# Optimization experiments

Measured on AMD Instinct MI355X. Metric: run time of the kernel, lower is better.

Reference implementation:

```python
import jax, jax.numpy as jnp
import numpy as np

N = 50000      # nodes
D = 16         # fixed in-degree per node
E = N * D      # edges
C = 128        # in_channels == hidden_channels
H = 128        # hidden_channels
ED = 16        # edge_dim
OUT = 2        # out_channels


def setup_inputs() -> dict:
    key = jax.random.key(0)
    ks = jax.random.split(key, 16)
    s = 0.05
    x = jax.random.normal(ks[0], (N, C), jnp.float32)
    src = jax.random.randint(ks[1], (E,), 0, N)
    dst = jnp.repeat(jnp.arange(N), D)           # sorted by destination, degree D each
    edge_index = jnp.stack([src, dst]).astype(jnp.int32)
    edge_attr = jax.random.normal(ks[2], (E, ED), jnp.float32)
    # 3 SAGEConv layers, each: LSTM(C->C) aggregator + lin_l(C->H, bias) + lin_r(C->H, no bias)
    Wih = jax.random.normal(ks[3], (3, 4 * C, C), jnp.float32) * s
    Whh = jax.random.normal(ks[4], (3, 4 * C, C), jnp.float32) * s
    bih = jax.random.normal(ks[5], (3, 4 * C), jnp.float32) * s
    bhh = jax.random.normal(ks[6], (3, 4 * C), jnp.float32) * s
    lin_l_W = jax.random.normal(ks[7], (3, H, C), jnp.float32) * s
    lin_l_b = jax.random.normal(ks[8], (3, H), jnp.float32) * s
    lin_r_W = jax.random.normal(ks[9], (3, H, C), jnp.float32) * s
    # edge MLP: (2H+ED)->H->H//2->OUT
    W1 = jax.random.normal(ks[10], (H, 2 * H + ED), jnp.float32) * s
    b1 = jax.random.normal(ks[11], (H,), jnp.float32) * s
    W2 = jax.random.normal(ks[12], (H // 2, H), jnp.float32) * s
    b2 = jax.random.normal(ks[13], (H // 2,), jnp.float32) * s
    W3 = jax.random.normal(ks[14], (OUT, H // 2), jnp.float32) * s
    b3 = jax.random.normal(ks[15], (OUT,), jnp.float32) * s
    return dict(x=x, edge_index=edge_index, edge_attr=edge_attr,
                Wih=Wih, Whh=Whh, bih=bih, bhh=bhh,
                lin_l_W=lin_l_W, lin_l_b=lin_l_b, lin_r_W=lin_r_W,
                W1=W1, b1=b1, W2=W2, b2=b2, W3=W3, b3=b3)


def _lstm_last(seq, wih, whh, bi, bh):
    # seq: [N, D, C] -> last LSTM output [N, C] (torch gate order i,f,g,o)
    h0 = jnp.zeros((seq.shape[0], whh.shape[1]), seq.dtype)

    def step(carry, xt):
        h, c = carry
        gates = xt @ wih.T + bi + h @ whh.T + bh
        i, f, g, o = jnp.split(gates, 4, axis=-1)
        c = jax.nn.sigmoid(f) * c + jax.nn.sigmoid(i) * jnp.tanh(g)
        h = jax.nn.sigmoid(o) * jnp.tanh(c)
        return (h, c), None

    (h, _), _ = jax.lax.scan(step, (h0, h0), seq.transpose(1, 0, 2))
    return h


def _sage_lstm(x, src, wih, whh, bi, bh, wl, bl, wr):
    # fixed degree D, edges sorted by dst -> group-by-dst is a reshape
    seq = x[src].reshape(N, D, -1)           # [N, D, C] neighbor sequences
    agg = _lstm_last(seq, wih, whh, bi, bh)  # [N, C]
    return agg @ wl.T + bl + x @ wr.T        # lin_l(agg) + lin_r(x)


def reference(x, edge_index, edge_attr, Wih, Whh, bih, bhh,
              lin_l_W, lin_l_b, lin_r_W, W1, b1, W2, b2, W3, b3):
    src, dst = edge_index[0], edge_index[1]
    h = x
    for l in range(3):
        h = jax.nn.relu(_sage_lstm(h, src, Wih[l], Whh[l], bih[l], bhh[l],
                                   lin_l_W[l], lin_l_b[l], lin_r_W[l]))
    # gather-concat edge MLP (dropout is identity in eval)
    feat = jnp.concatenate([h[src], h[dst], edge_attr], axis=1)  # [E, 2H+ED]
    e = jax.nn.relu(feat @ W1.T + b1)
    e = jax.nn.relu(e @ W2.T + b2)
    return e @ W3.T + b3
```

## Files before the change

### kernel.cpp

```cpp
#include <hip/hip_runtime.h>
#include <hip/hip_bf16.h>

#define NN 50000
#define DEG 16

typedef __attribute__((ext_vector_type(8))) short bfrag;
typedef __attribute__((ext_vector_type(4))) float f32x4;

__device__ __forceinline__ float bf2f(unsigned int u){ return __uint_as_float(u<<16); }
__device__ __forceinline__ unsigned short f2bf(float x){
  unsigned int u = __float_as_uint(x);
  unsigned int r = (u + 0x7fffu + ((u>>16)&1u)) >> 16;
  return (unsigned short)r;
}
__device__ __forceinline__ float fast_rcp(float x){ return __builtin_amdgcn_rcpf(x); }
__device__ __forceinline__ float sigmoidf_(float x){ return fast_rcp(1.f + __expf(-x)); }
__device__ __forceinline__ float tanh_fast(float x){
  float e = __expf(-2.f*fabsf(x));
  float r = (1.f - e)*fast_rcp(1.f + e);
  return copysignf(r, x);
}

#define SWZ(row) (((((row) ^ ((row)>>3)) & 7)) << 4)
#define SW4(row) (((row) & 15) << 4)

#define GLDS16(g, l) __builtin_amdgcn_global_load_lds( \
    (const __attribute__((address_space(1))) unsigned int*)(g), \
    (__attribute__((address_space(3))) unsigned int*)(l), 16, 0, 0)

__global__ void k_cvt(const float* __restrict__ in, unsigned short* __restrict__ out, int n){
  int i = blockIdx.x*256 + threadIdx.x;
  if (i < n) out[i] = f2bf(in[i]);
}

__global__ void k_cvt2(const float* __restrict__ in, unsigned short* __restrict__ out,
                       int stride, int off, int cols, int total){
  int i = blockIdx.x*256 + threadIdx.x;
  if (i < total){
    int r = i / cols, c = i - r*cols;
    out[i] = f2bf(in[(size_t)r*stride + off + c]);
  }
}

__global__ void k_prep_lstm(const float* __restrict__ Wih, const float* __restrict__ Whh,
                            const float* __restrict__ bih, const float* __restrict__ bhh,
                            unsigned short* __restrict__ Wcat, float* __restrict__ bsum)
{
  int i = blockIdx.x*256 + threadIdx.x;
  if (i < 3*512*256){
    int l = i >> 17;
    int rem = i & 131071;
    int row = rem >> 8, col = rem & 255;
    float v = (col < 128) ? Wih[((size_t)l*512 + row)*128 + col]
                          : Whh[((size_t)l*512 + row)*128 + (col-128)];
    Wcat[i] = f2bf(v);
  } else if (i < 3*512*256 + 3*512){
    int k = i - 3*512*256;
    bsum[k] = bih[k] + bhh[k];
  }
}

__global__ void k_prep_edge(const float* __restrict__ W1, const float* __restrict__ W2,
                            const float* __restrict__ W3,
                            unsigned short* __restrict__ W1eh, unsigned short* __restrict__ W1el,
                            unsigned short* __restrict__ W2h, unsigned short* __restrict__ W2l,
                            unsigned short* __restrict__ W3p)
{
  int i = blockIdx.x*256 + threadIdx.x;
  if (i < 8192){
    float v = W2[i];
    unsigned short hi = f2bf(v);
    W2h[i] = hi; W2l[i] = f2bf(v - bf2f(hi));
  } else if (i < 10240){
    int k = i - 8192; int j = k >> 4, kk = k & 15;
    float v = W1[(size_t)j*272 + 256 + kk];
    unsigned short hi = f2bf(v);
    W1eh[k] = hi; W1el[k] = f2bf(v - bf2f(hi));
  } else if (i < 11264){
    int k = i - 10240; int nr = k >> 6, c = k & 63;
    W3p[k] = f2bf(nr < 2 ? W3[nr*64 + c] : 0.f);
  }
}

__global__ __launch_bounds__(256,4) void k_bgemm(
    const unsigned short* __restrict__ Ab, const unsigned short* __restrict__ A2b,
    const unsigned short* __restrict__ Wb, const unsigned short* __restrict__ W2b,
    const float* __restrict__ bias, const float* __restrict__ bias2,
    float* __restrict__ outF, unsigned short* __restrict__ outB,
    int ostride, int dorelu, int n)
{
  const int t  = threadIdx.x;
  const int w  = t >> 6;
  const int l  = t & 63;
  const int ln = l & 15, q = l >> 4;
  const int n0 = blockIdx.x*64;
  const int j0 = blockIdx.y*128 + w*32;

  int nodeM[4];
#pragma unroll
  for (int mt=0;mt<4;mt++){ int nd = n0 + mt*16 + ln; nodeM[mt] = nd < n ? nd : n-1; }

  f32x4 acc[4][2];
#pragma unroll
  for (int mt=0;mt<4;mt++)
#pragma unroll
    for (int nt=0;nt<2;nt++) acc[mt][nt] = (f32x4){0.f,0.f,0.f,0.f};

  auto pass = [&](const unsigned short* __restrict__ Ap, const unsigned short* __restrict__ Wp){
#pragma unroll
    for (int ks=0;ks<4;ks++){
      bfrag Af[4], Bf[2];
#pragma unroll
      for (int mt=0;mt<4;mt++)
        Af[mt] = *(const bfrag*)(Ap + (size_t)nodeM[mt]*128 + ks*32 + q*8);
#pragma unroll
      for (int nt=0;nt<2;nt++)
        Bf[nt] = *(const bfrag*)(Wp + (size_t)(j0 + nt*16 + ln)*128 + ks*32 + q*8);
#pragma unroll
      for (int mt=0;mt<4;mt++)
#pragma unroll
        for (int nt=0;nt<2;nt++)
          acc[mt][nt] = __builtin_amdgcn_mfma_f32_16x16x32_bf16(Af[mt], Bf[nt], acc[mt][nt], 0,0,0);
    }
  };
  pass(Ab, Wb);
  if (A2b) pass(A2b, W2b);

#pragma unroll
  for (int nt=0;nt<2;nt++){
    int j = j0 + nt*16 + ln;
    float bv = bias ? bias[j] : 0.f;
    if (bias2) bv += bias2[j];
#pragma unroll
    for (int mt=0;mt<4;mt++)
#pragma unroll
      for (int r=0;r<4;r++){
        int row = n0 + mt*16 + q*4 + r;
        if (row < n){
          float v = acc[mt][nt][r] + bv;
          if (dorelu) v = fmaxf(v, 0.f);
          if (outF) outF[(size_t)row*ostride + j] = v;
          if (outB) outB[(size_t)row*ostride + j] = f2bf(v);
        }
      }
  }
}

__global__ __launch_bounds__(512,2) void k_lstm9(
    const unsigned short* __restrict__ xin,
    const int* __restrict__ src,
    const unsigned short* __restrict__ Wcat,
    const float* __restrict__ bsum,
    const unsigned short* __restrict__ Wlb,
    const unsigned short* __restrict__ Wrb,
    const float* __restrict__ bl,
    unsigned short* __restrict__ hout,
    int n)
{
  __shared__ unsigned short hs[64*128];
  __shared__ unsigned short xbuf[2][64*128];
  __shared__ int srcs[64*16];
  const int t  = threadIdx.x;
  const int w  = t >> 6;
  const int l  = t & 63;
  const int ln = l & 15;
  const int q  = l >> 4;
  const int n0 = blockIdx.x * 64;

  for (int i = t; i < 1024; i += 512){
    int nl = i >> 4, st = i & 15;
    srcs[i] = (n0+nl < n) ? src[(size_t)(n0+nl)*16 + st] : 0;
  }

  bfrag A[4][8];
#pragma unroll
  for (int T=0;T<4;T++)
#pragma unroll
    for (int ks=0;ks<8;ks++)
      A[T][ks] = *(const bfrag*)(Wcat + (size_t)(T*128 + w*16 + ln)*256 + ks*32 + q*8);

  f32x4 bsv[4];
#pragma unroll
  for (int T=0;T<4;T++)
    bsv[T] = *(const f32x4*)(bsum + T*128 + w*16 + q*4);

  float c[4][4];
#pragma unroll
  for (int nt=0;nt<4;nt++)
#pragma unroll
    for (int r=0;r<4;r++) c[nt][r]=0.f;

  __syncthreads();

  auto stageX = [&](int step, int buf){
#pragma unroll
    for (int j=0;j<2;j++){
      int row  = w*8 + j*4 + (l>>4);
      int node = srcs[row*16 + step];
      const char* gsrc = (const char*)xin + (size_t)node*256 + (((l&15)*16) ^ SW4(row));
      char* ldst = (char*)&xbuf[buf][0] + (w*8 + j*4)*256;
      GLDS16(gsrc, ldst);
    }
  };

  stageX(0, 0);
  asm volatile("s_waitcnt vmcnt(0)" ::: "memory");
  __syncthreads();

  for (int step=0; step<16; step++){
    const int cur = step & 1;
    if (step < 15) stageX(step+1, cur^1);

#pragma unroll
    for (int p=0;p<2;p++){
      f32x4 acc[4][2];
#pragma unroll
      for (int T=0;T<4;T++)
#pragma unroll
        for (int ntl=0;ntl<2;ntl++) acc[T][ntl] = (f32x4){0.f,0.f,0.f,0.f};

#pragma unroll
      for (int ntl=0; ntl<2; ntl++){
        int node = p*32 + ntl*16 + ln;
        int swz  = SW4(node);
#pragma unroll
        for (int ks=0;ks<4;ks++){
          bfrag Bk = *(const bfrag*)((const char*)&xbuf[cur][0] + node*256 +
                       ((ks*64 + q*16) ^ swz));
#pragma unroll
          for (int T=0;T<4;T++)
            acc[T][ntl] = __builtin_amdgcn_mfma_f32_16x16x32_bf16(A[T][ks], Bk, acc[T][ntl], 0,0,0);
        }
        if (step > 0){
#pragma unroll
          for (int ks=4;ks<8;ks++){
            bfrag Bk = *(const bfrag*)((const char*)hs + node*256 +
                         (((ks-4)*64 + q*16) ^ swz));
#pragma unroll
            for (int T=0;T<4;T++)
              acc[T][ntl] = __builtin_amdgcn_mfma_f32_16x16x32_bf16(A[T][ks], Bk, acc[T][ntl], 0,0,0);
          }
        }
      }

      if (p == 1){
        asm volatile("s_waitcnt vmcnt(0)" ::: "memory");
      }
      __syncthreads();

#pragma unroll
      for (int ntl=0; ntl<2; ntl++){
        int nt = p*2 + ntl;
        int node = p*32 + ntl*16 + ln;
        float h[4];
#pragma unroll
        for (int r=0;r<4;r++){
          float iv = acc[0][ntl][r] + bsv[0][r];
          float fv = acc[1][ntl][r] + bsv[1][r];
          float gg = acc[2][ntl][r] + bsv[2][r];
          float ov = acc[3][ntl][r] + bsv[3][r];
          float cn = sigmoidf_(fv)*c[nt][r] + sigmoidf_(iv)*tanh_fast(gg);
          c[nt][r] = cn;
          h[r] = sigmoidf_(ov)*tanh_fast(cn);
        }
        unsigned pk01, pk23;
        asm("v_cvt_pk_bf16_f32 %0, %1, %2" : "=v"(pk01) : "v"(h[0]), "v"(h[1]));
        asm("v_cvt_pk_bf16_f32 %0, %1, %2" : "=v"(pk23) : "v"(h[2]), "v"(h[3]));
        uint2 pv; pv.x = pk01; pv.y = pk23;
        *(uint2*)((char*)hs + node*256 + (((w*32 + q*8)) ^ SW4(node))) = pv;
      }
    }
  }

  __syncthreads();
  {
    bfrag Al[4], Ar[4];
#pragma unroll
    for (int ks=0;ks<4;ks++){
      Al[ks] = *(const bfrag*)(Wlb + (size_t)(w*16+ln)*128 + ks*32 + q*8);
      Ar[ks] = *(const bfrag*)(Wrb + (size_t)(w*16+ln)*128 + ks*32 + q*8);
    }
    f32x4 blv = *(const f32x4*)(bl + w*16 + q*4);
#pragma unroll
    for (int nt=0; nt<4; nt++){
      int node = nt*16 + ln;
      int gn = (n0+node < n) ? (n0+node) : (n-1);
      f32x4 acc = (f32x4){0.f,0.f,0.f,0.f};
#pragma unroll
      for (int ks=0;ks<4;ks++){
        bfrag Bh = *(const bfrag*)((const char*)hs + node*256 +
                     ((ks*64 + q*16) ^ SW4(node)));
        bfrag Bx = *(const bfrag*)(xin + (size_t)gn*128 + ks*32 + q*8);
        acc = __builtin_amdgcn_mfma_f32_16x16x32_bf16(Al[ks], Bh, acc, 0,0,0);
        acc = __builtin_amdgcn_mfma_f32_16x16x32_bf16(Ar[ks], Bx, acc, 0,0,0);
      }
      float v0 = fmaxf(acc[0]+blv[0], 0.f), v1 = fmaxf(acc[1]+blv[1], 0.f);
      float v2 = fmaxf(acc[2]+blv[2], 0.f), v3 = fmaxf(acc[3]+blv[3], 0.f);
      unsigned pk01, pk23;
      asm("v_cvt_pk_bf16_f32 %0, %1, %2" : "=v"(pk01) : "v"(v0), "v"(v1));
      asm("v_cvt_pk_bf16_f32 %0, %1, %2" : "=v"(pk23) : "v"(v2), "v"(v3));
      if (n0+node < n){
        uint2 pv; pv.x = pk01; pv.y = pk23;
        *(uint2*)(hout + (size_t)(n0+node)*128 + w*16 + q*4) = pv;
      }
    }
  }
}

__global__ __launch_bounds__(256,2) void k_edge3(
    const float* __restrict__ HsHd,
    const float* __restrict__ ea,
    const int* __restrict__ src,
    const unsigned short* __restrict__ W1eh, const unsigned short* __restrict__ W1el,
    const unsigned short* __restrict__ W2h,  const unsigned short* __restrict__ W2l,
    const unsigned short* __restrict__ W3p,
    const float* __restrict__ b1, const float* __restrict__ b2, const float* __restrict__ b3,
    float* __restrict__ out)
{
  __shared__ unsigned short out1h[64*128];
  __shared__ unsigned short out1l[64*128];
  __shared__ unsigned short e2h[64*64];
  __shared__ unsigned short e2l[64*64];
  __shared__ unsigned short ea2[64*56];

  const int t = threadIdx.x;
  const int w = t>>6, l = t&63, ln = l&15, q = l>>4;
  const int nblk = blockIdx.x;
  const size_t e0 = (size_t)nblk*64;

  int srcv[4];
#pragma unroll
  for (int r=0;r<4;r++) srcv[r] = src[e0 + w*16 + q*4 + r];

  float hsv[8][4];
#pragma unroll
  for (int nt=0;nt<8;nt++)
#pragma unroll
    for (int r=0;r<4;r++)
      hsv[nt][r] = HsHd[(size_t)srcv[r]*256 + nt*16 + ln];

  float hdv[8];
#pragma unroll
  for (int nt=0;nt<8;nt++)
    hdv[nt] = HsHd[((size_t)nblk*4 + w)*256 + 128 + nt*16 + ln];

  float b1v[8];
#pragma unroll
  for (int nt=0;nt<8;nt++) b1v[nt] = b1[nt*16 + ln];
  float b2v[4];
#pragma unroll
  for (int nt=0;nt<4;nt++) b2v[nt] = b2[nt*16 + ln];
  float b3v = (ln<2) ? b3[ln] : 0.f;

  bfrag w1h[8], w1l[8];
#pragma unroll
  for (int nt=0;nt<8;nt++){
    int j = nt*16 + ln;
    w1h[nt] = *(const bfrag*)(W1eh + (size_t)j*16 + (q&1)*8);
    w1l[nt] = *(const bfrag*)(W1el + (size_t)j*16 + (q&1)*8);
  }
  bfrag w3f[2];
#pragma unroll
  for (int ks=0;ks<2;ks++)
    w3f[ks] = *(const bfrag*)(W3p + (size_t)ln*64 + ks*32 + q*8);

  for (int i=t;i<1024;i+=256){
    int e=i>>4, k=i&15;
    float v = ea[(e0+e)*16 + k];
    unsigned short hi = f2bf(v);
    ea2[e*56 + k] = hi;
    ea2[e*56 + 16 + k] = f2bf(v - bf2f(hi));
  }
  __syncthreads();

  {
    bfrag Aea = *(const bfrag*)&ea2[(w*16+ln)*56 + q*8];
#pragma unroll
    for (int nt=0;nt<8;nt++){
      f32x4 acc;
#pragma unroll
      for (int r=0;r<4;r++) acc[r] = b1v[nt] + hdv[nt] + hsv[nt][r];
      acc = __builtin_amdgcn_mfma_f32_16x16x32_bf16(Aea, w1h[nt], acc, 0,0,0);
      acc = __builtin_amdgcn_mfma_f32_16x16x32_bf16(Aea, w1l[nt], acc, 0,0,0);
      int j = nt*16 + ln;
#pragma unroll
      for (int r=0;r<4;r++){
        int row = w*16 + q*4 + r;
        float v = fmaxf(acc[r], 0.f);
        unsigned short hi = f2bf(v);
        float lo = v - bf2f(hi);
        int byt = row*256 + ((j*2) ^ SWZ(row));
        *(unsigned short*)((char*)out1h + byt) = hi;
        *(unsigned short*)((char*)out1l + byt) = f2bf(lo);
      }
    }
  }
  __syncthreads();

  {
    f32x4 acc[4];
#pragma unroll
    for (int nt=0;nt<4;nt++) acc[nt] = (f32x4){b2v[nt],b2v[nt],b2v[nt],b2v[nt]};
    int arow = w*16 + ln;

    bfrag BhA[4], BlA[4], BhB[4], BlB[4];
#pragma unroll
    for (int nt=0;nt<4;nt++){
      int j = nt*16 + ln;
      BhA[nt] = *(const bfrag*)(W2h + (size_t)j*128 + q*8);
      BlA[nt] = *(const bfrag*)(W2l + (size_t)j*128 + q*8);
    }
#pragma unroll
    for (int ks=0;ks<4;ks++){
      if (ks < 3){
#pragma unroll
        for (int nt=0;nt<4;nt++){
          int j = nt*16 + ln;
          if ((ks&1)==0){
            BhB[nt] = *(const bfrag*)(W2h + (size_t)j*128 + (ks+1)*32 + q*8);
            BlB[nt] = *(const bfrag*)(W2l + (size_t)j*128 + (ks+1)*32 + q*8);
          } else {
            BhA[nt] = *(const bfrag*)(W2h + (size_t)j*128 + (ks+1)*32 + q*8);
            BlA[nt] = *(const bfrag*)(W2l + (size_t)j*128 + (ks+1)*32 + q*8);
          }
        }
      }
      int byt = arow*256 + ((ks*64 + q*16) ^ SWZ(arow));
      bfrag Ah = *(const bfrag*)((char*)out1h + byt);
      bfrag Al = *(const bfrag*)((char*)out1l + byt);
#pragma unroll
      for (int nt=0;nt<4;nt++){
        bfrag Bh = ((ks&1)==0) ? BhA[nt] : BhB[nt];
        bfrag Bl = ((ks&1)==0) ? BlA[nt] : BlB[nt];
        acc[nt] = __builtin_amdgcn_mfma_f32_16x16x32_bf16(Ah, Bh, acc[nt], 0,0,0);
        acc[nt] = __builtin_amdgcn_mfma_f32_16x16x32_bf16(Al, Bh, acc[nt], 0,0,0);
        acc[nt] = __builtin_amdgcn_mfma_f32_16x16x32_bf16(Ah, Bl, acc[nt], 0,0,0);
      }
    }
#pragma unroll
    for (int nt=0;nt<4;nt++)
#pragma unroll
      for (int r=0;r<4;r++){
        int row = w*16 + q*4 + r;
        int j = nt*16 + ln;
        float v = fmaxf(acc[nt][r], 0.f);
        unsigned short hi = f2bf(v);
        float lo = v - bf2f(hi);
        int byt = row*128 + ((j*2) ^ SWZ(row));
        *(unsigned short*)((char*)e2h + byt) = hi;
        *(unsigned short*)((char*)e2l + byt) = f2bf(lo);
      }
  }
  __syncthreads();

  {
    f32x4 acc = (f32x4){b3v,b3v,b3v,b3v};
    int arow = w*16 + ln;
#pragma unroll
    for (int ks=0;ks<2;ks++){
      int byt = arow*128 + ((ks*64 + q*16) ^ SWZ(arow));
      bfrag Ah = *(const bfrag*)((char*)e2h + byt);
      bfrag Al = *(const bfrag*)((char*)e2l + byt);
      acc = __builtin_amdgcn_mfma_f32_16x16x32_bf16(Ah, w3f[ks], acc, 0,0,0);
      acc = __builtin_amdgcn_mfma_f32_16x16x32_bf16(Al, w3f[ks], acc, 0,0,0);
    }
    if (ln < 2){
#pragma unroll
      for (int r=0;r<4;r++){
        int row = w*16 + q*4 + r;
        out[(e0 + row)*2 + ln] = acc[r];
      }
    }
  }
}

extern "C" void kernel_launch(void* const* d_in, const int* in_sizes, int n_in,
                              void* d_out, int out_size, void* d_ws, size_t ws_size,
                              hipStream_t stream) {
  const float* x    = (const float*)d_in[0];
  const int*   eidx = (const int*)  d_in[1];
  const float* eatt = (const float*)d_in[2];
  const float* Wih  = (const float*)d_in[3];
  const float* Whh  = (const float*)d_in[4];
  const float* bih  = (const float*)d_in[5];
  const float* bhh  = (const float*)d_in[6];
  const float* WlL  = (const float*)d_in[7];
  const float* blL  = (const float*)d_in[8];
  const float* WrL  = (const float*)d_in[9];
  const float* W1   = (const float*)d_in[10];
  const float* b1   = (const float*)d_in[11];
  const float* W2   = (const float*)d_in[12];
  const float* b2   = (const float*)d_in[13];
  const float* W3   = (const float*)d_in[14];
  const float* b3   = (const float*)d_in[15];
  const int*   src  = eidx;

  char* p = (char*)d_ws;
  float* HsHd        = (float*)p;
  p += (size_t)NN*512*2;
  unsigned short* xb   = (unsigned short*)p; p += (size_t)NN*128*2;
  unsigned short* hb1  = (unsigned short*)p; p += (size_t)NN*128*2;
  unsigned short* hb2  = (unsigned short*)p; p += (size_t)NN*128*2;
  unsigned short* Wcat = (unsigned short*)p; p += (size_t)3*512*256*2;
  float* bsum          = (float*)p;          p += (size_t)3*512*4;
  unsigned short* Wlb  = (unsigned short*)p; p += (size_t)3*128*128*2;
  unsigned short* Wrb  = (unsigned short*)p; p += (size_t)3*128*128*2;
  unsigned short* W1nb = (unsigned short*)p; p += (size_t)256*128*2;
  unsigned short* W1eh = (unsigned short*)p; p += 2048*2;
  unsigned short* W1el = (unsigned short*)p; p += 2048*2;
  unsigned short* W2h  = (unsigned short*)p; p += 8192*2;
  unsigned short* W2l  = (unsigned short*)p; p += 8192*2;
  unsigned short* W3p  = (unsigned short*)p; p += 1024*2;

  dim3 blk(256);
  const int nb = (NN + 63)/64;

  k_cvt<<<(NN*128+255)/256, blk, 0, stream>>>(x, xb, NN*128);
  k_prep_lstm<<<(3*512*256 + 3*512 + 255)/256, blk, 0, stream>>>(Wih, Whh, bih, bhh, Wcat, bsum);
  k_cvt<<<(3*128*128+255)/256, blk, 0, stream>>>(WlL, Wlb, 3*128*128);
  k_cvt<<<(3*128*128+255)/256, blk, 0, stream>>>(WrL, Wrb, 3*128*128);
  k_cvt2<<<(128*128+255)/256, blk, 0, stream>>>(W1, W1nb,           272, 0,   128, 128*128);
  k_cvt2<<<(128*128+255)/256, blk, 0, stream>>>(W1, W1nb+128*128,   272, 128, 128, 128*128);
  k_prep_edge<<<(11264+255)/256, blk, 0, stream>>>(W1, W2, W3, W1eh, W1el, W2h, W2l, W3p);

  const unsigned short* hin = xb;
  unsigned short* houts[3] = {hb1, hb2, hb1};
  for (int l = 0; l < 3; l++){
    k_lstm9<<<dim3(nb),dim3(512),0,stream>>>(hin, src,
        Wcat + (size_t)l*512*256, bsum + (size_t)l*512,
        Wlb + (size_t)l*128*128, Wrb + (size_t)l*128*128, blL + (size_t)l*128,
        houts[l], NN);
    hin = houts[l];
  }
  k_bgemm<<<dim3(nb,2),blk,0,stream>>>(hin, nullptr, W1nb, nullptr,
                                       nullptr, nullptr, HsHd, nullptr, 256, 0, NN);
  k_edge3<<<dim3(NN/4),blk,0,stream>>>(HsHd, eatt, src, W1eh, W1el, W2h, W2l, W3p,
                                       b1, b2, b3, (float*)d_out);
}
```

Before: 1.394 ms.

## Store node projections as bf16 and merge weight-prep kernels into one launch

The node-level W1 projection (HsHd) is now written by the bgemm as bf16 instead of fp32, and the edge kernel gathers bf16 values and widens them in registers. This halves the bytes of the random src gather and of the dst reads in the edge MLP. Separately, the six small weight-conversion launches are folded into one kernel to cut launch overhead. The bf16 rounding of the pre-activation projections adds numerical error to the first edge-MLP layer.

```diff
diff --git a/kernel.cpp b/kernel.cpp
--- a/kernel.cpp
+++ b/kernel.cpp
@@ -33,51 +33,53 @@
   if (i < n) out[i] = f2bf(in[i]);
 }
 
-__global__ void k_cvt2(const float* __restrict__ in, unsigned short* __restrict__ out,
-                       int stride, int off, int cols, int total){
-  int i = blockIdx.x*256 + threadIdx.x;
-  if (i < total){
-    int r = i / cols, c = i - r*cols;
-    out[i] = f2bf(in[(size_t)r*stride + off + c]);
-  }
-}
-
-__global__ void k_prep_lstm(const float* __restrict__ Wih, const float* __restrict__ Whh,
-                            const float* __restrict__ bih, const float* __restrict__ bhh,
-                            unsigned short* __restrict__ Wcat, float* __restrict__ bsum)
+__global__ void k_prep_all(const float* __restrict__ Wih, const float* __restrict__ Whh,
+                           const float* __restrict__ bih, const float* __restrict__ bhh,
+                           const float* __restrict__ WlL, const float* __restrict__ WrL,
+                           const float* __restrict__ W1,  const float* __restrict__ W2,
+                           const float* __restrict__ W3,
+                           unsigned short* __restrict__ Wcat, float* __restrict__ bsum,
+                           unsigned short* __restrict__ Wlb,  unsigned short* __restrict__ Wrb,
+                           unsigned short* __restrict__ W1nb,
+                           unsigned short* __restrict__ W1eh, unsigned short* __restrict__ W1el,
+                           unsigned short* __restrict__ W2h,  unsigned short* __restrict__ W2l,
+                           unsigned short* __restrict__ W3p)
 {
   int i = blockIdx.x*256 + threadIdx.x;
-  if (i < 3*512*256){
+  if (i < 393216){
     int l = i >> 17;
     int rem = i & 131071;
     int row = rem >> 8, col = rem & 255;
     float v = (col < 128) ? Wih[((size_t)l*512 + row)*128 + col]
                           : Whh[((size_t)l*512 + row)*128 + (col-128)];
     Wcat[i] = f2bf(v);
-  } else if (i < 3*512*256 + 3*512){
-    int k = i - 3*512*256;
+  } else if (i < 394752){
+    int k = i - 393216;
     bsum[k] = bih[k] + bhh[k];
-  }
-}
-
-__global__ void k_prep_edge(const float* __restrict__ W1, const float* __restrict__ W2,
-                            const float* __restrict__ W3,
-                            unsigned short* __restrict__ W1eh, unsigned short* __restrict__ W1el,
-                            unsigned short* __restrict__ W2h, unsigned short* __restrict__ W2l,
-                            unsigned short* __restrict__ W3p)
-{
-  int i = blockIdx.x*256 + threadIdx.x;
-  if (i < 8192){
-    float v = W2[i];
+  } else if (i < 443904){
+    int k = i - 394752;
+    Wlb[k] = f2bf(WlL[k]);
+  } else if (i < 493056){
+    int k = i - 443904;
+    Wrb[k] = f2bf(WrL[k]);
+  } else if (i < 509440){
+    int k = i - 493056; int r = k >> 7, c = k & 127;
+    W1nb[k] = f2bf(W1[(size_t)r*272 + c]);
+  } else if (i < 525824){
+    int k = i - 509440; int r = k >> 7, c = k & 127;
+    W1nb[16384 + k] = f2bf(W1[(size_t)r*272 + 128 + c]);
+  } else if (i < 534016){
+    int k = i - 525824;
+    float v = W2[k];
     unsigned short hi = f2bf(v);
-    W2h[i] = hi; W2l[i] = f2bf(v - bf2f(hi));
-  } else if (i < 10240){
-    int k = i - 8192; int j = k >> 4, kk = k & 15;
+    W2h[k] = hi; W2l[k] = f2bf(v - bf2f(hi));
+  } else if (i < 536064){
+    int k = i - 534016; int j = k >> 4, kk = k & 15;
     float v = W1[(size_t)j*272 + 256 + kk];
     unsigned short hi = f2bf(v);
     W1eh[k] = hi; W1el[k] = f2bf(v - bf2f(hi));
-  } else if (i < 11264){
-    int k = i - 10240; int nr = k >> 6, c = k & 63;
+  } else if (i < 537088){
+    int k = i - 536064; int nr = k >> 6, c = k & 63;
     W3p[k] = f2bf(nr < 2 ? W3[nr*64 + c] : 0.f);
   }
 }
@@ -307,8 +309,8 @@
   }
 }
 
-__global__ __launch_bounds__(256,2) void k_edge3(
-    const float* __restrict__ HsHd,
+__global__ __launch_bounds__(256,2) void k_edge4(
+    const unsigned short* __restrict__ HsHd,
     const float* __restrict__ ea,
     const int* __restrict__ src,
     const unsigned short* __restrict__ W1eh, const unsigned short* __restrict__ W1el,
@@ -332,17 +334,17 @@
 #pragma unroll
   for (int r=0;r<4;r++) srcv[r] = src[e0 + w*16 + q*4 + r];
 
-  float hsv[8][4];
+  unsigned short hsq[8][4];
 #pragma unroll
   for (int nt=0;nt<8;nt++)
 #pragma unroll
     for (int r=0;r<4;r++)
-      hsv[nt][r] = HsHd[(size_t)srcv[r]*256 + nt*16 + ln];
-
-  float hdv[8];
+      hsq[nt][r] = HsHd[(size_t)srcv[r]*256 + nt*16 + ln];
+
+  unsigned short hdq[8];
 #pragma unroll
   for (int nt=0;nt<8;nt++)
-    hdv[nt] = HsHd[((size_t)nblk*4 + w)*256 + 128 + nt*16 + ln];
+    hdq[nt] = HsHd[((size_t)nblk*4 + w)*256 + 128 + nt*16 + ln];
 
   float b1v[8];
 #pragma unroll
@@ -377,9 +379,10 @@
     bfrag Aea = *(const bfrag*)&ea2[(w*16+ln)*56 + q*8];
 #pragma unroll
     for (int nt=0;nt<8;nt++){
+      float hdv = bf2f((unsigned)hdq[nt]);
       f32x4 acc;
 #pragma unroll
-      for (int r=0;r<4;r++) acc[r] = b1v[nt] + hdv[nt] + hsv[nt][r];
+      for (int r=0;r<4;r++) acc[r] = b1v[nt] + hdv + bf2f((unsigned)hsq[nt][r]);
       acc = __builtin_amdgcn_mfma_f32_16x16x32_bf16(Aea, w1h[nt], acc, 0,0,0);
       acc = __builtin_amdgcn_mfma_f32_16x16x32_bf16(Aea, w1l[nt], acc, 0,0,0);
       int j = nt*16 + ln;
@@ -496,7 +499,7 @@
   const int*   src  = eidx;
 
   char* p = (char*)d_ws;
-  float* HsHd        = (float*)p;
+  unsigned short* HsHdB = (unsigned short*)p;
   p += (size_t)NN*512*2;
   unsigned short* xb   = (unsigned short*)p; p += (size_t)NN*128*2;
   unsigned short* hb1  = (unsigned short*)p; p += (size_t)NN*128*2;
@@ -516,12 +519,9 @@
   const int nb = (NN + 63)/64;
 
   k_cvt<<<(NN*128+255)/256, blk, 0, stream>>>(x, xb, NN*128);
-  k_prep_lstm<<<(3*512*256 + 3*512 + 255)/256, blk, 0, stream>>>(Wih, Whh, bih, bhh, Wcat, bsum);
-  k_cvt<<<(3*128*128+255)/256, blk, 0, stream>>>(WlL, Wlb, 3*128*128);
-  k_cvt<<<(3*128*128+255)/256, blk, 0, stream>>>(WrL, Wrb, 3*128*128);
-  k_cvt2<<<(128*128+255)/256, blk, 0, stream>>>(W1, W1nb,           272, 0,   128, 128*128);
-  k_cvt2<<<(128*128+255)/256, blk, 0, stream>>>(W1, W1nb+128*128,   272, 128, 128, 128*128);
-  k_prep_edge<<<(11264+255)/256, blk, 0, stream>>>(W1, W2, W3, W1eh, W1el, W2h, W2l, W3p);
+  k_prep_all<<<(537088+255)/256, blk, 0, stream>>>(Wih, Whh, bih, bhh, WlL, WrL, W1, W2, W3,
+                                                   Wcat, bsum, Wlb, Wrb, W1nb,
+                                                   W1eh, W1el, W2h, W2l, W3p);
 
   const unsigned short* hin = xb;
   unsigned short* houts[3] = {hb1, hb2, hb1};
@@ -533,7 +533,7 @@
     hin = houts[l];
   }
   k_bgemm<<<dim3(nb,2),blk,0,stream>>>(hin, nullptr, W1nb, nullptr,
-                                       nullptr, nullptr, HsHd, nullptr, 256, 0, NN);
-  k_edge3<<<dim3(NN/4),blk,0,stream>>>(HsHd, eatt, src, W1eh, W1el, W2h, W2l, W3p,
+                                       nullptr, nullptr, nullptr, HsHdB, 256, 0, NN);
+  k_edge4<<<dim3(NN/4),blk,0,stream>>>(HsHdB, eatt, src, W1eh, W1el, W2h, W2l, W3p,
                                        b1, b2, b3, (float*)d_out);
 }
```

Result: no change. 1.382 ms (-0.9%).
